# Kernel tuning notes

Hardware: AMD Instinct MI355X
Metric: run time of the kernel (lower is better)

The kernel has to match this reference:

```python
import jax, jax.numpy as jnp
import numpy as np

N_SLOTS, KEY_DIM, VAL_DIM = 8192, 64, 64
B, S, TOPK = 8, 2048, 8


def setup_inputs() -> dict:
    key = jax.random.key(0)
    k1, k2, k3, k4, k5 = jax.random.split(key, 5)
    queries = jax.random.normal(k1, (B, S, KEY_DIM), dtype=jnp.float32)
    keys_mem = jax.random.normal(k2, (N_SLOTS, KEY_DIM), dtype=jnp.float32) * 0.02
    vals_mem = jax.random.normal(k3, (N_SLOTS, VAL_DIM), dtype=jnp.float32) * 0.02
    fast_vals = jax.random.normal(k4, (N_SLOTS, VAL_DIM), dtype=jnp.float32) * 0.01
    timestamps = jax.random.uniform(k5, (N_SLOTS,), dtype=jnp.float32)
    return {
        "queries": queries,
        "keys_mem": keys_mem,
        "vals_mem": vals_mem,
        "fast_vals": fast_vals,
        "timestamps": timestamps,
        "topk": TOPK,
    }


def reference(queries, keys_mem, vals_mem, fast_vals, timestamps, topk):
    # sim: [B, S, n_slots], scaled dot-product vs. memory keys
    scale = keys_mem.shape[1] ** (-0.5)
    sim = jnp.einsum("bsd,nd->bsn", queries, keys_mem) * scale
    # topk indices computed on detached scores (torch uses sim.detach())
    _, idx = jax.lax.top_k(jax.lax.stop_gradient(sim), topk)  # idx: [B, S, k]
    # gather topk similarities (torch does this via one-hot * sim; same math)
    sim_topk = jnp.take_along_axis(sim, idx, axis=-1)  # [B, S, k]
    # effective memory = slow + fast store; gather rows (torch: one_hot @ memory)
    effective_memory = vals_mem + fast_vals  # [n_slots, val_dim]
    gathered_vals = effective_memory[idx]  # [B, S, k, val_dim]
    attn_weights = jax.nn.softmax(sim_topk, axis=-1)  # [B, S, k]
    weighted_vals = gathered_vals * attn_weights[..., None]  # [B, S, k, val_dim]
    ts_retrieved = timestamps[idx]  # [B, S, k]
    return weighted_vals, idx, ts_retrieved
```

## Files before the change

kernel.cpp:

```cpp
#include <hip/hip_runtime.h>
#include <math.h>

#define NQ      16384
#define NSLOTS  8192
#define D       64
#define K       8

#define WV_ELEMS  (NQ * K * D)
#define IDX_OFF   (WV_ELEMS)
#define TSO_OFF   (IDX_OFF + NQ * K)

#define QPB    32
#define BLOCK  512
#define WAVES  8
#define SPW    (NSLOTS / WAVES)
#define ITERS  (SPW / 32)

using short8  = __attribute__((ext_vector_type(8))) short;
using bf16x8  = __attribute__((ext_vector_type(8))) __bf16;
using f32x4   = __attribute__((ext_vector_type(4))) float;

#define MFMA_BF16(A, B, C) __builtin_amdgcn_mfma_f32_16x16x32_bf16((A), (B), (C), 0, 0, 0)

__device__ __forceinline__ bf16x8 load_frag(const unsigned short* p) {
    short8 s = *reinterpret_cast<const short8*>(p);
    return __builtin_bit_cast(bf16x8, s);
}

__device__ __forceinline__ float packkey(float s, int code) {
    unsigned u = __float_as_uint(s) & 0xFFFFE000u;
    return __uint_as_float(u | (unsigned)code);
}

__device__ __forceinline__ void ins8(float (&tv)[8], float key) {
    float k2 = fmaxf(key, tv[0]);
    float o0 = fminf(tv[1], k2);
    float o1 = __builtin_amdgcn_fmed3f(tv[1], tv[2], k2);
    float o2 = __builtin_amdgcn_fmed3f(tv[2], tv[3], k2);
    float o3 = __builtin_amdgcn_fmed3f(tv[3], tv[4], k2);
    float o4 = __builtin_amdgcn_fmed3f(tv[4], tv[5], k2);
    float o5 = __builtin_amdgcn_fmed3f(tv[5], tv[6], k2);
    float o6 = __builtin_amdgcn_fmed3f(tv[6], tv[7], k2);
    float o7 = fmaxf(tv[7], k2);
    tv[0]=o0; tv[1]=o1; tv[2]=o2; tv[3]=o3; tv[4]=o4; tv[5]=o5; tv[6]=o6; tv[7]=o7;
}

__device__ __forceinline__ void cs(float& a, float& b) {
    const float lo = fminf(a, b), hi = fmaxf(a, b);
    a = lo; b = hi;
}
__device__ __forceinline__ void sort_bitonic8(float (&v)[8]) {
    cs(v[0],v[4]); cs(v[1],v[5]); cs(v[2],v[6]); cs(v[3],v[7]);
    cs(v[0],v[2]); cs(v[1],v[3]); cs(v[4],v[6]); cs(v[5],v[7]);
    cs(v[0],v[1]); cs(v[2],v[3]); cs(v[4],v[5]); cs(v[6],v[7]);
}

__device__ __forceinline__ void csu(unsigned long long& a, unsigned long long& b) {
    const bool lt = a < b;
    const unsigned long long lo = lt ? a : b;
    const unsigned long long hi = lt ? b : a;
    a = lo; b = hi;
}
__device__ __forceinline__ void sort_bitonic8_u64(unsigned long long (&v)[8]) {
    csu(v[0],v[4]); csu(v[1],v[5]); csu(v[2],v[6]); csu(v[3],v[7]);
    csu(v[0],v[2]); csu(v[1],v[3]); csu(v[4],v[6]); csu(v[5],v[7]);
    csu(v[0],v[1]); csu(v[2],v[3]); csu(v[4],v[5]); csu(v[6],v[7]);
}

__device__ __forceinline__ unsigned short f2bf(float f) {
    unsigned u = __float_as_uint(f);
    return (unsigned short)((u + 0x7FFFu + ((u >> 16) & 1u)) >> 16);
}

__global__ __launch_bounds__(256)
void conv_kernel(const float* __restrict__ q, const float* __restrict__ k,
                 unsigned short* __restrict__ ws) {
    const int t = blockIdx.x * blockDim.x + threadIdx.x;
    if (t < 262144) {
        float4 v = reinterpret_cast<const float4*>(q)[t];
        unsigned long long r =
              (unsigned long long)f2bf(v.x * 0.125f)
            | ((unsigned long long)f2bf(v.y * 0.125f) << 16)
            | ((unsigned long long)f2bf(v.z * 0.125f) << 32)
            | ((unsigned long long)f2bf(v.w * 0.125f) << 48);
        reinterpret_cast<unsigned long long*>(ws + 524288)[t] = r;
    } else if (t < 393216) {
        const int i = t - 262144;
        float4 v = reinterpret_cast<const float4*>(k)[i];
        unsigned long long r =
              (unsigned long long)f2bf(v.x)
            | ((unsigned long long)f2bf(v.y) << 16)
            | ((unsigned long long)f2bf(v.z) << 32)
            | ((unsigned long long)f2bf(v.w) << 48);
        reinterpret_cast<unsigned long long*>(ws)[i] = r;
    }
}

__global__ __launch_bounds__(BLOCK, 4)
void ltm_mfma_kernel(const float* __restrict__ queries,
                     const float* __restrict__ keys_mem,
                     const float* __restrict__ vals_mem,
                     const float* __restrict__ fast_vals,
                     const float* __restrict__ timestamps,
                     const unsigned short* __restrict__ kb,
                     const unsigned short* __restrict__ qb,
                     float* __restrict__ out)
{
    __shared__ float candk[QPB][68];

    const int tid  = threadIdx.x;
    const int lane = tid & 63;
    const int w    = tid >> 6;
    const int row  = lane & 15;
    const int g    = lane >> 4;
    const int g4   = g * 4;
    const int koff = g * 8;
    const int qbase = blockIdx.x * QPB;

    const unsigned short* qpA = qb + (size_t)(qbase + row) * D + koff;
    const bf16x8 bA0 = load_frag(qpA);
    const bf16x8 bA1 = load_frag(qpA + 32);
    const bf16x8 bB0 = load_frag(qpA + 16 * D);
    const bf16x8 bB1 = load_frag(qpA + 16 * D + 32);

    float tvA[8], tvB[8];
    #pragma unroll
    for (int i = 0; i < 8; ++i) { tvA[i] = -INFINITY; tvB[i] = -INFINITY; }

    const int wbase = w * SPW;
    const unsigned short* kp0 = kb + (size_t)(wbase + row) * D + koff;
    bf16x8 a00 = load_frag(kp0);
    bf16x8 a01 = load_frag(kp0 + 32);
    bf16x8 a10 = load_frag(kp0 + 16 * D);
    bf16x8 a11 = load_frag(kp0 + 16 * D + 32);

    int codeA = 8191 - (wbase + g4);

    #pragma unroll 2
    for (int it = 0; it < ITERS; ++it) {
        const int snext = wbase + (it + 1) * 32;
        const unsigned short* np_ = kb + (size_t)(snext + row) * D + koff;
        bf16x8 n00 = load_frag(np_);
        bf16x8 n01 = load_frag(np_ + 32);
        bf16x8 n10 = load_frag(np_ + 16 * D);
        bf16x8 n11 = load_frag(np_ + 16 * D + 32);

        const f32x4 z = {0.f, 0.f, 0.f, 0.f};
        f32x4 c00 = MFMA_BF16(a00, bA0, z);  c00 = MFMA_BF16(a01, bA1, c00);
        f32x4 c01 = MFMA_BF16(a00, bB0, z);  c01 = MFMA_BF16(a01, bB1, c01);
        f32x4 c10 = MFMA_BF16(a10, bA0, z);  c10 = MFMA_BF16(a11, bA1, c10);
        f32x4 c11 = MFMA_BF16(a10, bB0, z);  c11 = MFMA_BF16(a11, bB1, c11);

        ins8(tvA, packkey(c00[0], codeA     ));
        ins8(tvA, packkey(c00[1], codeA -  1));
        ins8(tvA, packkey(c00[2], codeA -  2));
        ins8(tvA, packkey(c00[3], codeA -  3));
        ins8(tvA, packkey(c10[0], codeA - 16));
        ins8(tvA, packkey(c10[1], codeA - 17));
        ins8(tvA, packkey(c10[2], codeA - 18));
        ins8(tvA, packkey(c10[3], codeA - 19));
        ins8(tvB, packkey(c01[0], codeA     ));
        ins8(tvB, packkey(c01[1], codeA -  1));
        ins8(tvB, packkey(c01[2], codeA -  2));
        ins8(tvB, packkey(c01[3], codeA -  3));
        ins8(tvB, packkey(c11[0], codeA - 16));
        ins8(tvB, packkey(c11[1], codeA - 17));
        ins8(tvB, packkey(c11[2], codeA - 18));
        ins8(tvB, packkey(c11[3], codeA - 19));

        codeA -= 32;
        a00 = n00; a01 = n01; a10 = n10; a11 = n11;
    }

    {
        float sA[8], sB[8];
        #pragma unroll
        for (int j = 0; j < 8; ++j) {
            sA[j] = __shfl_xor(tvA[j], 32, 64);
            sB[j] = __shfl_xor(tvB[j], 32, 64);
        }
        float mA[8], mB[8];
        #pragma unroll
        for (int j = 0; j < 8; ++j) {
            mA[j] = fmaxf(tvA[j], sA[7 - j]);
            mB[j] = fmaxf(tvB[j], sB[7 - j]);
        }
        sort_bitonic8(mA);
        sort_bitonic8(mB);
        #pragma unroll
        for (int j = 0; j < 8; ++j) {
            sA[j] = __shfl_xor(mA[j], 16, 64);
            sB[j] = __shfl_xor(mB[j], 16, 64);
        }
        if (g == 0) {
            #pragma unroll
            for (int j = 0; j < 8; ++j) {
                candk[row     ][w * 8 + j] = fmaxf(mA[j], sA[7 - j]);
                candk[row + 16][w * 8 + j] = fmaxf(mB[j], sB[7 - j]);
            }
        }
    }
    __syncthreads();

    const int ql  = tid >> 4;
    const int l16 = tid & 15;
    const int sg  = l16 >> 2;
    const int ls4 = l16 & 3;
    const int q   = qbase + ql;

    float4 qv4[4];
    {
        const float4* qp = reinterpret_cast<const float4*>(queries) + (size_t)q * 16 + ls4 * 4;
        #pragma unroll
        for (int i = 0; i < 4; ++i) qv4[i] = qp[i];
    }

    unsigned long long tk[8];
    #pragma unroll
    for (int i = 0; i < 8; ++i) tk[i] = 0ull;

    #pragma unroll 4
    for (int jt = 0; jt < 16; ++jt) {
        const float fk  = candk[ql][sg * 16 + jt];
        const int   sid = 8191 - (int)(__float_as_uint(fk) & 8191u);
        const float4* kp = reinterpret_cast<const float4*>(keys_mem) + (size_t)sid * 16 + ls4 * 4;
        float p = 0.f;
        #pragma unroll
        for (int i = 0; i < 4; ++i) {
            const float4 kc = kp[i];
            p = fmaf(qv4[i].x, kc.x, p);
            p = fmaf(qv4[i].y, kc.y, p);
            p = fmaf(qv4[i].z, kc.z, p);
            p = fmaf(qv4[i].w, kc.w, p);
        }
        p += __shfl_xor(p, 1, 64);
        p += __shfl_xor(p, 2, 64);
        const float s = p * 0.125f;
        const unsigned u  = __float_as_uint(s);
        const unsigned ou = (u & 0x80000000u) ? ~u : (u | 0x80000000u);
        const unsigned long long key =
            ((unsigned long long)ou << 13) | (unsigned)(8191 - sid);
        if (key > tk[0]) {
            tk[0] = key;
            #pragma unroll
            for (int uu = 0; uu < 7; ++uu) {
                const bool sw = tk[uu] > tk[uu + 1];
                const unsigned long long x = sw ? tk[uu + 1] : tk[uu];
                const unsigned long long y = sw ? tk[uu]     : tk[uu + 1];
                tk[uu] = x; tk[uu + 1] = y;
            }
        }
    }

    #pragma unroll
    for (int st = 4; st <= 8; st <<= 1) {
        unsigned long long sk[8], mk[8];
        #pragma unroll
        for (int j = 0; j < 8; ++j) sk[j] = __shfl_xor(tk[j], st, 64);
        #pragma unroll
        for (int j = 0; j < 8; ++j) {
            const unsigned long long a = tk[j], b = sk[7 - j];
            mk[j] = a > b ? a : b;
        }
        sort_bitonic8_u64(mk);
        #pragma unroll
        for (int j = 0; j < 8; ++j) tk[j] = mk[j];
    }

    float wv[K]; int wi[K];
    #pragma unroll
    for (int r = 0; r < K; ++r) {
        const unsigned long long best = tk[7 - r];
        const int      sid = 8191 - (int)(best & 8191ull);
        const unsigned ou  = (unsigned)(best >> 13);
        const unsigned ub  = (ou & 0x80000000u) ? (ou & 0x7FFFFFFFu) : ~ou;
        wv[r] = __uint_as_float(ub);
        wi[r] = sid;
    }
    const float m = wv[0];
    float e[K]; float sum = 0.f;
    #pragma unroll
    for (int r = 0; r < K; ++r) { e[r] = expf(wv[r] - m); sum += e[r]; }
    const float inv = 1.f / sum;

    {
        const int   r   = l16 >> 1;
        const int   h   = l16 & 1;
        const int   id  = wi[r];
        const float wgt = e[r] * inv;
        const float4* vp = reinterpret_cast<const float4*>(vals_mem)  + (size_t)id * 16 + h * 8;
        const float4* fp = reinterpret_cast<const float4*>(fast_vals) + (size_t)id * 16 + h * 8;
        float4* op = reinterpret_cast<float4*>(out) + ((size_t)(q * K + r)) * 16 + h * 8;
        #pragma unroll
        for (int i = 0; i < 8; ++i) {
            const float4 a = vp[i];
            const float4 b = fp[i];
            float4 c;
            c.x = (a.x + b.x) * wgt;
            c.y = (a.y + b.y) * wgt;
            c.z = (a.z + b.z) * wgt;
            c.w = (a.w + b.w) * wgt;
            op[i] = c;
        }
        if (l16 < 8) {
            out[IDX_OFF + (size_t)q * K + l16] = (float)wi[l16];
        } else {
            const int r2 = l16 - 8;
            out[TSO_OFF + (size_t)q * K + r2] = timestamps[wi[r2]];
        }
    }
}

#define FQPB   32
#define FTPQ   8
#define FBLOCK 256
#define FTS    128
#define FLDK   68
#define FNTILES (NSLOTS / FTS)

__global__ __launch_bounds__(FBLOCK, 2)
void ltm_fused_kernel(const float* __restrict__ queries,
                      const float* __restrict__ keys_mem,
                      const float* __restrict__ vals_mem,
                      const float* __restrict__ fast_vals,
                      const float* __restrict__ timestamps,
                      float* __restrict__ out)
{
    __shared__ float kt[FTS * FLDK];
    __shared__ float candv[FQPB][FTPQ * K];
    __shared__ int   candi[FQPB][FTPQ * K];
    __shared__ float selw[FQPB][K];
    __shared__ int   seli[FQPB][K];

    const int tid = threadIdx.x;
    const int ql  = tid / FTPQ;
    const int sub = tid % FTPQ;
    const int q   = blockIdx.x * FQPB + ql;

    float4 qv[D / 4];
    {
        const float4* qp = reinterpret_cast<const float4*>(queries + (size_t)q * D);
        #pragma unroll
        for (int i = 0; i < D / 4; ++i) qv[i] = qp[i];
    }

    float tv[K]; int ti[K];
    #pragma unroll
    for (int i = 0; i < K; ++i) { tv[i] = -INFINITY; ti[i] = 0; }

    for (int tile = 0; tile < FNTILES; ++tile) {
        __syncthreads();
        {
            const float4* kg = reinterpret_cast<const float4*>(keys_mem + (size_t)tile * FTS * D);
            #pragma unroll
            for (int i = 0; i < (FTS * D / 4) / FBLOCK; ++i) {
                const int e = tid + i * FBLOCK;
                const int row = e >> 4;
                const int col = e & 15;
                *reinterpret_cast<float4*>(&kt[row * FLDK + col * 4]) = kg[e];
            }
        }
        __syncthreads();

        #pragma unroll 4
        for (int j = 0; j < FTS / FTPQ; ++j) {
            const int local = sub + j * FTPQ;
            const float* kr = &kt[local * FLDK];
            float4 a0 = make_float4(0.f, 0.f, 0.f, 0.f);
            float4 a1 = make_float4(0.f, 0.f, 0.f, 0.f);
            #pragma unroll
            for (int i = 0; i < D / 4; i += 2) {
                const float4 k0 = *reinterpret_cast<const float4*>(&kr[(i + 0) * 4]);
                const float4 k1 = *reinterpret_cast<const float4*>(&kr[(i + 1) * 4]);
                a0.x = fmaf(k0.x, qv[i].x, a0.x);   a0.y = fmaf(k0.y, qv[i].y, a0.y);
                a0.z = fmaf(k0.z, qv[i].z, a0.z);   a0.w = fmaf(k0.w, qv[i].w, a0.w);
                a1.x = fmaf(k1.x, qv[i+1].x, a1.x); a1.y = fmaf(k1.y, qv[i+1].y, a1.y);
                a1.z = fmaf(k1.z, qv[i+1].z, a1.z); a1.w = fmaf(k1.w, qv[i+1].w, a1.w);
            }
            float s = ((a0.x + a1.x) + (a0.y + a1.y)) + ((a0.z + a1.z) + (a0.w + a1.w));
            s *= 0.125f;
            const int gid = tile * FTS + local;
            if (s > tv[0]) {
                tv[0] = s; ti[0] = gid;
                #pragma unroll
                for (int u = 0; u < K - 1; ++u) {
                    const bool sw = tv[u] > tv[u + 1];
                    const float va = sw ? tv[u + 1] : tv[u];
                    const float vb = sw ? tv[u]     : tv[u + 1];
                    const int   ia = sw ? ti[u + 1] : ti[u];
                    const int   ib = sw ? ti[u]     : ti[u + 1];
                    tv[u] = va; tv[u + 1] = vb; ti[u] = ia; ti[u + 1] = ib;
                }
            }
        }
    }

    #pragma unroll
    for (int i = 0; i < K; ++i) {
        candv[ql][sub * K + i] = tv[i];
        candi[ql][sub * K + i] = ti[i];
    }
    __syncthreads();

    if (sub == 0) {
        float wv[K]; int wi[K];
        #pragma unroll
        for (int r = 0; r < K; ++r) {
            float bv = -INFINITY; int bi = 0x7fffffff; int bp = 0;
            for (int c = 0; c < FTPQ * K; ++c) {
                const float v = candv[ql][c];
                const int  id = candi[ql][c];
                if ((v > bv) || (v == bv && id < bi)) { bv = v; bi = id; bp = c; }
            }
            candv[ql][bp] = -INFINITY;
            wv[r] = bv; wi[r] = bi;
        }
        const float m = wv[0];
        float e[K]; float sum = 0.f;
        #pragma unroll
        for (int r = 0; r < K; ++r) { e[r] = expf(wv[r] - m); sum += e[r]; }
        const float inv = 1.f / sum;
        #pragma unroll
        for (int r = 0; r < K; ++r) { selw[ql][r] = e[r] * inv; seli[ql][r] = wi[r]; }
    }
    __syncthreads();

    {
        const int r = sub;
        const int id = seli[ql][r];
        const float w = selw[ql][r];
        const float4* vp = reinterpret_cast<const float4*>(vals_mem  + (size_t)id * D);
        const float4* fp = reinterpret_cast<const float4*>(fast_vals + (size_t)id * D);
        float4* op = reinterpret_cast<float4*>(out + (size_t)(q * K + r) * D);
        #pragma unroll
        for (int i = 0; i < D / 4; ++i) {
            const float4 a = vp[i];
            const float4 b = fp[i];
            float4 c;
            c.x = (a.x + b.x) * w; c.y = (a.y + b.y) * w;
            c.z = (a.z + b.z) * w; c.w = (a.w + b.w) * w;
            op[i] = c;
        }
        out[IDX_OFF + (size_t)q * K + r] = (float)id;
        out[TSO_OFF + (size_t)q * K + r] = timestamps[id];
    }
}

extern "C" void kernel_launch(void* const* d_in, const int* in_sizes, int n_in,
                              void* d_out, int out_size, void* d_ws, size_t ws_size,
                              hipStream_t stream) {
    (void)in_sizes; (void)n_in; (void)out_size;
    const float* queries    = (const float*)d_in[0];
    const float* keys_mem   = (const float*)d_in[1];
    const float* vals_mem   = (const float*)d_in[2];
    const float* fast_vals  = (const float*)d_in[3];
    const float* timestamps = (const float*)d_in[4];
    float* out = (float*)d_out;

    if (ws_size >= (size_t)3 * 1024 * 1024) {
        unsigned short* ws = (unsigned short*)d_ws;
        conv_kernel<<<1536, 256, 0, stream>>>(queries, keys_mem, ws);
        ltm_mfma_kernel<<<NQ / QPB, BLOCK, 0, stream>>>(
            queries, keys_mem, vals_mem, fast_vals, timestamps,
            ws , ws + 524288 , out);
    } else {
        ltm_fused_kernel<<<NQ / FQPB, FBLOCK, 0, stream>>>(
            queries, keys_mem, vals_mem, fast_vals, timestamps, out);
    }
}
```

Before: 109.5 us.

## Split top-k into bf16 MFMA prefilter over slot halves plus fp32 rescore kernel

Replaces the single fused MFMA top-k kernel with two kernels. The first uses bf16 MFMA over half the slots per block (twice as many blocks, higher occupancy bound) and writes a top-16 candidate pool per half. The second rescores the 32 candidates per query in exact fp32, picks the final top-8, and writes the softmax-weighted values, indices and timestamps. This is meant to raise parallelism in the scoring pass and to recover exact fp32 ordering cheaply. In exchange it adds a kernel launch and a workspace round trip, and it needs a larger workspace to take this path.

```diff
diff --git a/kernel.cpp b/kernel.cpp
--- a/kernel.cpp
+++ b/kernel.cpp
@@ -10,15 +10,23 @@
 #define IDX_OFF   (WV_ELEMS)
 #define TSO_OFF   (IDX_OFF + NQ * K)
 
-#define QPB    32
-#define BLOCK  512
-#define WAVES  8
-#define SPW    (NSLOTS / WAVES)
-#define ITERS  (SPW / 32)
-
-using short8  = __attribute__((ext_vector_type(8))) short;
-using bf16x8  = __attribute__((ext_vector_type(8))) __bf16;
-using f32x4   = __attribute__((ext_vector_type(4))) float;
+#define QPB_P   32
+#define BLOCK_P 512
+#define HALVES  2
+#define SPW_P   (NSLOTS / HALVES / 8)
+#define ITERS_P (SPW_P / 32)
+
+#define QPB_R   16
+#define BLOCK_R 256
+
+#define POOL_SHORT_OFF 1572864
+#define WS_NEED_NEW  (4u * 1024u * 1024u)
+#define WS_NEED_OLD  (3u * 1024u * 1024u)
+
+using short8   = __attribute__((ext_vector_type(8))) short;
+using ushort8  = __attribute__((ext_vector_type(8))) unsigned short;
+using bf16x8   = __attribute__((ext_vector_type(8))) __bf16;
+using f32x4    = __attribute__((ext_vector_type(4))) float;
 
 #define MFMA_BF16(A, B, C) __builtin_amdgcn_mfma_f32_16x16x32_bf16((A), (B), (C), 0, 0, 0)
 
@@ -95,6 +103,281 @@
         reinterpret_cast<unsigned long long*>(ws)[i] = r;
     }
 }
+
+__global__ __launch_bounds__(BLOCK_P, 8)
+void ltm_prefilter_kernel(const unsigned short* __restrict__ kb,
+                          const unsigned short* __restrict__ qb,
+                          unsigned short* __restrict__ poolu)
+{
+    __shared__ float candk[QPB_P][68];
+
+    const int tid  = threadIdx.x;
+    const int lane = tid & 63;
+    const int w    = tid >> 6;
+    const int row  = lane & 15;
+    const int g    = lane >> 4;
+    const int g4   = g * 4;
+    const int koff = g * 8;
+    const int bid  = blockIdx.x;
+    const int qbase = (bid >> 1) * QPB_P;
+    const int half  = bid & 1;
+
+    const unsigned short* qpA = qb + (size_t)(qbase + row) * D + koff;
+    const bf16x8 bA0 = load_frag(qpA);
+    const bf16x8 bA1 = load_frag(qpA + 32);
+    const bf16x8 bB0 = load_frag(qpA + 16 * D);
+    const bf16x8 bB1 = load_frag(qpA + 16 * D + 32);
+
+    float tvA[8], tvB[8];
+    #pragma unroll
+    for (int i = 0; i < 8; ++i) { tvA[i] = -INFINITY; tvB[i] = -INFINITY; }
+
+    const int wbase = half * (NSLOTS / HALVES) + w * SPW_P;
+    int codeA = 8191 - (wbase + g4);
+
+    for (int it = 0; it < ITERS_P; ++it) {
+        const int s0 = wbase + it * 32;
+        const unsigned short* p = kb + (size_t)(s0 + row) * D + koff;
+        const bf16x8 a00 = load_frag(p);
+        const bf16x8 a01 = load_frag(p + 32);
+        const bf16x8 a10 = load_frag(p + 16 * D);
+        const bf16x8 a11 = load_frag(p + 16 * D + 32);
+
+        const f32x4 z = {0.f, 0.f, 0.f, 0.f};
+        f32x4 c00 = MFMA_BF16(a00, bA0, z);  c00 = MFMA_BF16(a01, bA1, c00);
+        f32x4 c01 = MFMA_BF16(a00, bB0, z);  c01 = MFMA_BF16(a01, bB1, c01);
+        f32x4 c10 = MFMA_BF16(a10, bA0, z);  c10 = MFMA_BF16(a11, bA1, c10);
+        f32x4 c11 = MFMA_BF16(a10, bB0, z);  c11 = MFMA_BF16(a11, bB1, c11);
+
+        ins8(tvA, packkey(c00[0], codeA     ));
+        ins8(tvA, packkey(c00[1], codeA -  1));
+        ins8(tvA, packkey(c00[2], codeA -  2));
+        ins8(tvA, packkey(c00[3], codeA -  3));
+        ins8(tvA, packkey(c10[0], codeA - 16));
+        ins8(tvA, packkey(c10[1], codeA - 17));
+        ins8(tvA, packkey(c10[2], codeA - 18));
+        ins8(tvA, packkey(c10[3], codeA - 19));
+        ins8(tvB, packkey(c01[0], codeA     ));
+        ins8(tvB, packkey(c01[1], codeA -  1));
+        ins8(tvB, packkey(c01[2], codeA -  2));
+        ins8(tvB, packkey(c01[3], codeA -  3));
+        ins8(tvB, packkey(c11[0], codeA - 16));
+        ins8(tvB, packkey(c11[1], codeA - 17));
+        ins8(tvB, packkey(c11[2], codeA - 18));
+        ins8(tvB, packkey(c11[3], codeA - 19));
+
+        codeA -= 32;
+    }
+
+    {
+        float sA[8], sB[8];
+        #pragma unroll
+        for (int j = 0; j < 8; ++j) {
+            sA[j] = __shfl_xor(tvA[j], 32, 64);
+            sB[j] = __shfl_xor(tvB[j], 32, 64);
+        }
+        float mA[8], mB[8];
+        #pragma unroll
+        for (int j = 0; j < 8; ++j) {
+            mA[j] = fmaxf(tvA[j], sA[7 - j]);
+            mB[j] = fmaxf(tvB[j], sB[7 - j]);
+        }
+        sort_bitonic8(mA);
+        sort_bitonic8(mB);
+        #pragma unroll
+        for (int j = 0; j < 8; ++j) {
+            sA[j] = __shfl_xor(mA[j], 16, 64);
+            sB[j] = __shfl_xor(mB[j], 16, 64);
+        }
+        float fA[8], fB[8];
+        #pragma unroll
+        for (int j = 0; j < 8; ++j) {
+            fA[j] = fmaxf(mA[j], sA[7 - j]);
+            fB[j] = fmaxf(mB[j], sB[7 - j]);
+        }
+        sort_bitonic8(fA);
+        sort_bitonic8(fB);
+        if (g == 0) {
+            #pragma unroll
+            for (int j = 0; j < 8; ++j) {
+                candk[row     ][w * 8 + j] = fA[j];
+                candk[row + 16][w * 8 + j] = fB[j];
+            }
+        }
+    }
+    __syncthreads();
+
+    if (tid < 256) {
+        const int  ql = tid >> 3;
+        const int  jj = tid & 7;
+        const bool hi = (jj & 1) != 0;
+
+        float v[8];
+        #pragma unroll
+        for (int i = 0; i < 8; ++i) v[i] = candk[ql][jj * 8 + i];
+
+        {
+            float sk[8], mk[8];
+            #pragma unroll
+            for (int i = 0; i < 8; ++i) sk[i] = __shfl_xor(v[i], 1, 64);
+            #pragma unroll
+            for (int i = 0; i < 8; ++i)
+                mk[i] = hi ? fmaxf(v[i], sk[7 - i]) : fminf(v[i], sk[7 - i]);
+            sort_bitonic8(mk);
+            #pragma unroll
+            for (int i = 0; i < 8; ++i) v[i] = mk[i];
+        }
+        #pragma unroll
+        for (int rnd = 0; rnd < 2; ++rnd) {
+            const int st = rnd ? 5 : 3;
+            float sk[8], mk[8], sk2[8];
+            #pragma unroll
+            for (int i = 0; i < 8; ++i) sk[i] = __shfl_xor(v[i], st, 64);
+            #pragma unroll
+            for (int i = 0; i < 8; ++i) mk[i] = fmaxf(v[i], sk[7 - i]);
+            #pragma unroll
+            for (int i = 0; i < 8; ++i) sk2[i] = __shfl_xor(mk[i], 1, 64);
+            #pragma unroll
+            for (int i = 0; i < 8; ++i)
+                mk[i] = hi ? fmaxf(mk[i], sk2[i]) : fminf(mk[i], sk2[i]);
+            sort_bitonic8(mk);
+            #pragma unroll
+            for (int i = 0; i < 8; ++i) v[i] = mk[i];
+        }
+        if (jj < 2) {
+            ushort8 o;
+            #pragma unroll
+            for (int i = 0; i < 8; ++i)
+                o[i] = (unsigned short)(8191u - (__float_as_uint(v[i]) & 8191u));
+            *reinterpret_cast<ushort8*>(
+                poolu + ((size_t)(qbase + ql) * 32 + half * 16 + jj * 8)) = o;
+        }
+    }
+}
+
+__global__ __launch_bounds__(BLOCK_R, 4)
+void ltm_rescore_kernel(const float* __restrict__ queries,
+                        const float* __restrict__ keys_mem,
+                        const float* __restrict__ vals_mem,
+                        const float* __restrict__ fast_vals,
+                        const float* __restrict__ timestamps,
+                        const unsigned short* __restrict__ poolu,
+                        float* __restrict__ out)
+{
+    const int tid = threadIdx.x;
+    const int ql  = tid >> 4;
+    const int l16 = tid & 15;
+    const int sg  = l16 >> 2;
+    const int ls4 = l16 & 3;
+    const int q   = blockIdx.x * QPB_R + ql;
+
+    float4 qv4[4];
+    {
+        const float4* qp = reinterpret_cast<const float4*>(queries) + (size_t)q * 16 + ls4 * 4;
+        #pragma unroll
+        for (int i = 0; i < 4; ++i) qv4[i] = qp[i];
+    }
+
+    unsigned long long tk[8];
+    #pragma unroll
+    for (int i = 0; i < 8; ++i) tk[i] = 0ull;
+
+    #pragma unroll 4
+    for (int jt = 0; jt < 8; ++jt) {
+        const int sid = poolu[(size_t)q * 32 + sg * 8 + jt];
+        const float4* kp = reinterpret_cast<const float4*>(keys_mem) + (size_t)sid * 16 + ls4 * 4;
+        float p = 0.f;
+        #pragma unroll
+        for (int i = 0; i < 4; ++i) {
+            const float4 kc = kp[i];
+            p = fmaf(qv4[i].x, kc.x, p);
+            p = fmaf(qv4[i].y, kc.y, p);
+            p = fmaf(qv4[i].z, kc.z, p);
+            p = fmaf(qv4[i].w, kc.w, p);
+        }
+        p += __shfl_xor(p, 1, 64);
+        p += __shfl_xor(p, 2, 64);
+        const float s = p * 0.125f;
+        const unsigned u  = __float_as_uint(s);
+        const unsigned ou = (u & 0x80000000u) ? ~u : (u | 0x80000000u);
+        const unsigned long long key =
+            ((unsigned long long)ou << 13) | (unsigned)(8191 - sid);
+        if (key > tk[0]) {
+            tk[0] = key;
+            #pragma unroll
+            for (int uu = 0; uu < 7; ++uu) {
+                const bool sw = tk[uu] > tk[uu + 1];
+                const unsigned long long x = sw ? tk[uu + 1] : tk[uu];
+                const unsigned long long y = sw ? tk[uu]     : tk[uu + 1];
+                tk[uu] = x; tk[uu + 1] = y;
+            }
+        }
+    }
+
+    #pragma unroll
+    for (int st = 4; st <= 8; st <<= 1) {
+        unsigned long long sk[8], mk[8];
+        #pragma unroll
+        for (int j = 0; j < 8; ++j) sk[j] = __shfl_xor(tk[j], st, 64);
+        #pragma unroll
+        for (int j = 0; j < 8; ++j) {
+            const unsigned long long a = tk[j], b = sk[7 - j];
+            mk[j] = a > b ? a : b;
+        }
+        sort_bitonic8_u64(mk);
+        #pragma unroll
+        for (int j = 0; j < 8; ++j) tk[j] = mk[j];
+    }
+
+    float wv[K]; int wi[K];
+    #pragma unroll
+    for (int r = 0; r < K; ++r) {
+        const unsigned long long best = tk[7 - r];
+        const int      sid = 8191 - (int)(best & 8191ull);
+        const unsigned ou  = (unsigned)(best >> 13);
+        const unsigned ub  = (ou & 0x80000000u) ? (ou & 0x7FFFFFFFu) : ~ou;
+        wv[r] = __uint_as_float(ub);
+        wi[r] = sid;
+    }
+    const float m = wv[0];
+    float e[K]; float sum = 0.f;
+    #pragma unroll
+    for (int r = 0; r < K; ++r) { e[r] = expf(wv[r] - m); sum += e[r]; }
+    const float inv = 1.f / sum;
+
+    {
+        const int   r   = l16 >> 1;
+        const int   h   = l16 & 1;
+        const int   id  = wi[r];
+        const float wgt = e[r] * inv;
+        const float4* vp = reinterpret_cast<const float4*>(vals_mem)  + (size_t)id * 16 + h * 8;
+        const float4* fp = reinterpret_cast<const float4*>(fast_vals) + (size_t)id * 16 + h * 8;
+        float4* op = reinterpret_cast<float4*>(out) + ((size_t)(q * K + r)) * 16 + h * 8;
+        #pragma unroll
+        for (int i = 0; i < 8; ++i) {
+            const float4 a = vp[i];
+            const float4 b = fp[i];
+            float4 c;
+            c.x = (a.x + b.x) * wgt;
+            c.y = (a.y + b.y) * wgt;
+            c.z = (a.z + b.z) * wgt;
+            c.w = (a.w + b.w) * wgt;
+            op[i] = c;
+        }
+        if (l16 < 8) {
+            out[IDX_OFF + (size_t)q * K + l16] = (float)wi[l16];
+        } else {
+            const int r2 = l16 - 8;
+            out[TSO_OFF + (size_t)q * K + r2] = timestamps[wi[r2]];
+        }
+    }
+}
+
+#define QPB    32
+#define BLOCK  512
+#define WAVES  8
+#define SPW    (NSLOTS / WAVES)
+#define ITERS  (SPW / 32)
 
 __global__ __launch_bounds__(BLOCK, 4)
 void ltm_mfma_kernel(const float* __restrict__ queries,
@@ -457,7 +740,15 @@
     const float* timestamps = (const float*)d_in[4];
     float* out = (float*)d_out;
 
-    if (ws_size >= (size_t)3 * 1024 * 1024) {
+    if (ws_size >= WS_NEED_NEW) {
+        unsigned short* ws = (unsigned short*)d_ws;
+        unsigned short* poolu = ws + POOL_SHORT_OFF;
+        conv_kernel<<<1536, 256, 0, stream>>>(queries, keys_mem, ws);
+        ltm_prefilter_kernel<<<(NQ / QPB_P) * HALVES, BLOCK_P, 0, stream>>>(
+            ws , ws + 524288 , poolu);
+        ltm_rescore_kernel<<<NQ / QPB_R, BLOCK_R, 0, stream>>>(
+            queries, keys_mem, vals_mem, fast_vals, timestamps, poolu, out);
+    } else if (ws_size >= WS_NEED_OLD) {
         unsigned short* ws = (unsigned short*)d_ws;
         conv_kernel<<<1536, 256, 0, stream>>>(queries, keys_mem, ws);
         ltm_mfma_kernel<<<NQ / QPB, BLOCK, 0, stream>>>(
```

Result: slower. 112.2 us (+2.4%).
